# Kernel tuning notes

Hardware: AMD Instinct MI355X
Metric: run time of the kernel (lower is better)

## Reference

```python
import jax, jax.numpy as jnp
import numpy as np


def setup_inputs() -> dict:
    key = jax.random.key(0)
    k1, k2, k3, k4 = jax.random.split(key, 4)
    B, C = 32768, 10
    x = jax.random.normal(k1, (B, 1, 28, 28), dtype=jnp.float32)
    linear_weight = jax.random.normal(k2, (4 * 14 * 14 + 1 + 2, C), dtype=jnp.float32)
    linear_bias = jax.random.normal(k3, (C,), dtype=jnp.float32)
    sampler_weights = jax.random.normal(k4, (4,), dtype=jnp.float32)
    return {"x": x, "linear_weight": linear_weight, "linear_bias": linear_bias,
            "sampler_weights": sampler_weights}


def reference(x, linear_weight, linear_bias, sampler_weights):
    # Closed-form simulation of the 4-qubit circuits:
    # RY(t)|0> -> <Z>=cos(t); after CX(0,1): <Z1> = cos(t0)*cos(t1); CX(2,3) likewise.
    B = x.shape[0]
    # Extract non-overlapping 2x2 patches in row-major order -> (B, 196, 4)
    p = x[:, 0].reshape(B, 14, 2, 14, 2).transpose(0, 1, 3, 2, 4).reshape(B, 196, 4)
    c = jnp.cos(p)
    # quanvolution_circuit per patch: [cos a, cos a cos b, cos c, cos c cos d]
    feats = jnp.stack([c[..., 0], c[..., 0] * c[..., 1],
                       c[..., 2], c[..., 2] * c[..., 3]], axis=-1)  # (B,196,4)
    qfeat = feats.reshape(B, 784)
    # fully_connected_circuit on qfeat[:, :4]: mean of the four post-CX <Z>
    cf = jnp.cos(qfeat[:, :4])
    qfc = (cf[:, 0] + cf[:, 0] * cf[:, 1] + cf[:, 2] + cf[:, 2] * cf[:, 3]) / 4.0  # (B,)
    # sampler_circuit: sequential RY angles add on wires 0 and 1
    t0 = qfeat[:, 0] + sampler_weights[0] + sampler_weights[2]
    t1 = qfeat[:, 1] + sampler_weights[1] + sampler_weights[3]
    z0 = jnp.cos(t0)
    z1 = z0 * jnp.cos(t1)
    sampler = jax.nn.softmax(jnp.stack([z0, z1], axis=-1), axis=-1)  # (B,2)
    combined = jnp.concatenate([qfeat, qfc[:, None], sampler], axis=-1)  # (B,787)
    logits = combined @ linear_weight + linear_bias
    return jax.nn.log_softmax(logits, axis=-1)
```

## Files before the change

kernel.cpp:

```cpp
#include <hip/hip_runtime.h>


__global__ __launch_bounds__(256, 8)
void qml_k1(const float* __restrict__ x,
            const float* __restrict__ wm,
            float* __restrict__ part,
            float* __restrict__ qf,
            int B, int nblk)
{
    __shared__ float red[3][64 * 11];

    const int lane = threadIdx.x & 63;
    const int wv = __builtin_amdgcn_readfirstlane((int)(threadIdx.x >> 6));
    const int g = blockIdx.x;
    const int ps = blockIdx.y;

    int sample = g * 64 + lane;
    const bool s_ok = (sample < B);
    if (sample >= B) sample = B - 1;
    const float* __restrict__ xrow = x + (size_t)sample * 784;

    const int i = 2 * ps + (wv >> 1);
    const int j = 7 * (wv & 1);
    const int p0 = i * 14 + j;
    const int xoff = i * 56 + 2 * j;

    float acc[10];
#pragma unroll
    for (int c = 0; c < 10; ++c) acc[c] = 0.0f;

    float q0 = 0.f, q1 = 0.f, q2 = 0.f, q3 = 0.f;

#pragma unroll
    for (int t = 0; t < 7; ++t) {
        const float2 a01 = *(const float2*)(xrow + xoff + 2 * t);
        const float2 a23 = *(const float2*)(xrow + xoff + 28 + 2 * t);

        const float c0 = __cosf(a01.x);
        const float c1 = __cosf(a01.y);
        const float c2 = __cosf(a23.x);
        const float c3 = __cosf(a23.y);
        const float v0 = c0;
        const float v1 = c0 * c1;
        const float v2 = c2;
        const float v3 = c2 * c3;

        if (t == 0 && ps == 0 && wv == 0) { q0 = v0; q1 = v1; q2 = v2; q3 = v3; }

        const float* __restrict__ wr = wm + 40 * (p0 + t);
#pragma unroll
        for (int c = 0; c < 10; ++c)
            acc[c] += v0 * wr[c] + v1 * wr[10 + c] + v2 * wr[20 + c] + v3 * wr[30 + c];
    }

    if (ps == 0 && wv == 0 && s_ok) {
        float* __restrict__ qd = qf + 4 * (size_t)sample;
        qd[0] = q0; qd[1] = q1; qd[2] = q2; qd[3] = q3;
    }

    if (wv != 0) {
#pragma unroll
        for (int c = 0; c < 10; ++c) red[wv - 1][lane * 11 + c] = acc[c];
    }
    __syncthreads();

    if (wv == 0) {
        float* __restrict__ dst = part + ((size_t)(ps * nblk + g)) * 640 + lane * 10;
#pragma unroll
        for (int c = 0; c < 10; ++c)
            dst[c] = acc[c] + red[0][lane * 11 + c] + red[1][lane * 11 + c]
                            + red[2][lane * 11 + c];
    }
}

__global__ __launch_bounds__(640, 1)
void qml_k2(const float* __restrict__ part,
            const float* __restrict__ qf,
            const float* __restrict__ wm,
            const float* __restrict__ bias,
            const float* __restrict__ sw,
            float* __restrict__ out,
            int B, int nblk)
{
    __shared__ float lg[64 * 11];

    const int t = threadIdx.x;
    const int g = blockIdx.x;
    const int s = t / 10;
    const int c = t - 10 * s;

    float sum = 0.0f;
#pragma unroll
    for (int ps = 0; ps < 7; ++ps)
        sum += part[((size_t)(ps * nblk + g)) * 640 + t];

    int sample = g * 64 + s;
    const bool ok = (sample < B);
    if (sample >= B) sample = B - 1;

    const float* __restrict__ qr = qf + 4 * (size_t)sample;
    const float q0 = qr[0], q1 = qr[1], q2 = qr[2], q3 = qr[3];

    const float f0 = __cosf(q0), f1 = __cosf(q1);
    const float f2 = __cosf(q2), f3 = __cosf(q3);
    const float qfc = (f0 + f0 * f1 + f2 + f2 * f3) * 0.25f;

    const float t0 = q0 + sw[0] + sw[2];
    const float t1 = q1 + sw[1] + sw[3];
    const float z0 = __cosf(t0);
    const float z1 = z0 * __cosf(t1);
    const float e0 = __expf(z0);
    const float e1 = __expf(z1);
    const float inv = 1.0f / (e0 + e1);
    const float s0 = e0 * inv, s1 = e1 * inv;

    const float* __restrict__ wt = wm + 7840;
    const float logit = sum + bias[c] + qfc * wt[c] + s0 * wt[10 + c] + s1 * wt[20 + c];
    lg[s * 11 + c] = logit;
    __syncthreads();

    float m = -3.4e38f;
#pragma unroll
    for (int k = 0; k < 10; ++k) m = fmaxf(m, lg[s * 11 + k]);
    float ssum = 0.0f;
#pragma unroll
    for (int k = 0; k < 10; ++k) ssum += __expf(lg[s * 11 + k] - m);
    const float lse = __logf(ssum) + m;

    if (ok) out[(size_t)g * 640 + t] = logit - lse;
}

extern "C" void kernel_launch(void* const* d_in, const int* in_sizes, int n_in,
                              void* d_out, int out_size, void* d_ws, size_t ws_size,
                              hipStream_t stream) {
    const float* x    = (const float*)d_in[0];
    const float* w    = (const float*)d_in[1];
    const float* bias = (const float*)d_in[2];
    const float* sw   = (const float*)d_in[3];
    float* out = (float*)d_out;

    const int B = in_sizes[0] / 784;
    const int nblk = (B + 63) / 64;

    float* part = (float*)d_ws;
    float* qf   = part + (size_t)7 * nblk * 640;

    dim3 grid1(nblk, 7);
    qml_k1<<<grid1, 256, 0, stream>>>(x, w, part, qf, B, nblk);
    qml_k2<<<nblk, 640, 0, stream>>>(part, qf, w, bias, sw, out, B, nblk);
}
```

Measured before the change: 181.8 us.

## Stage input rows through swizzled LDS with coalesced loads and transpose partial layouts

Each block now loads its 64 samples' 4-row slab with coalesced float4 reads into XOR-swizzled shared memory, instead of per-lane strided float2 reads straight from global memory. The partial sums and the qf features are stored column-major so that writes and reads in both kernels coalesce. The second kernel is remapped to match, and an extra LDS pass produces the output row-major. This replaces uncoalesced global traffic, at the cost of 32KB of LDS per block and a lower occupancy hint (launch bounds 5 instead of 8).

Result: faster. 165.0 us (-9.3%).

```diff
diff --git a/kernel.cpp b/kernel.cpp
--- a/kernel.cpp
+++ b/kernel.cpp
@@ -1,75 +1,98 @@
 #include <hip/hip_runtime.h>
 
 
-__global__ __launch_bounds__(256, 8)
+__global__ __launch_bounds__(256, 5)
 void qml_k1(const float* __restrict__ x,
             const float* __restrict__ wm,
             float* __restrict__ part,
             float* __restrict__ qf,
             int B, int nblk)
 {
-    __shared__ float red[3][64 * 11];
+    __shared__ float lds[64 * 128];
 
-    const int lane = threadIdx.x & 63;
-    const int wv = __builtin_amdgcn_readfirstlane((int)(threadIdx.x >> 6));
+    const int t = threadIdx.x;
+    const int lane = t & 63;
+    const int wv = __builtin_amdgcn_readfirstlane((int)(t >> 6));
     const int g = blockIdx.x;
     const int ps = blockIdx.y;
 
-    int sample = g * 64 + lane;
-    const bool s_ok = (sample < B);
-    if (sample >= B) sample = B - 1;
-    const float* __restrict__ xrow = x + (size_t)sample * 784;
+    {
+        const int base_s = g * 64;
+#pragma unroll
+        for (int k = 0; k < 7; ++k) {
+            const int f = k * 256 + t;
+            const int s = f / 28;
+            const int c = f - 28 * s;
+            int sg = base_s + s; if (sg >= B) sg = B - 1;
+            const float4 v = *(const float4*)(x + (size_t)sg * 784 + ps * 112 + 4 * c);
+            const int m2 = (s & 15) << 1;
+            float* __restrict__ d0 = lds + s * 128 + ((4 * c) ^ m2);
+            float* __restrict__ d1 = lds + s * 128 + ((4 * c + 2) ^ m2);
+            *(float2*)d0 = make_float2(v.x, v.y);
+            *(float2*)d1 = make_float2(v.z, v.w);
+        }
+    }
+    __syncthreads();
 
-    const int i = 2 * ps + (wv >> 1);
-    const int j = 7 * (wv & 1);
-    const int p0 = i * 14 + j;
-    const int xoff = i * 56 + 2 * j;
+    const int i_loc = wv >> 1;
+    const int jbase = 7 * (wv & 1);
+    const int o_top = i_loc * 56 + 2 * jbase;
+    const int p0 = (2 * ps + i_loc) * 14 + jbase;
+    const int m2 = (lane & 15) << 1;
+    const float* __restrict__ row = lds + lane * 128;
 
     float acc[10];
 #pragma unroll
     for (int c = 0; c < 10; ++c) acc[c] = 0.0f;
-
     float q0 = 0.f, q1 = 0.f, q2 = 0.f, q3 = 0.f;
 
 #pragma unroll
-    for (int t = 0; t < 7; ++t) {
-        const float2 a01 = *(const float2*)(xrow + xoff + 2 * t);
-        const float2 a23 = *(const float2*)(xrow + xoff + 28 + 2 * t);
+    for (int tt = 0; tt < 7; ++tt) {
+        const int ot = o_top + 2 * tt;
+        const float2 a = *(const float2*)(row + (ot ^ m2));
+        const float2 b = *(const float2*)(row + ((ot + 28) ^ m2));
 
-        const float c0 = __cosf(a01.x);
-        const float c1 = __cosf(a01.y);
-        const float c2 = __cosf(a23.x);
-        const float c3 = __cosf(a23.y);
-        const float v0 = c0;
-        const float v1 = c0 * c1;
-        const float v2 = c2;
-        const float v3 = c2 * c3;
+        const float c0 = __cosf(a.x);
+        const float c1 = __cosf(a.y);
+        const float c2 = __cosf(b.x);
+        const float c3 = __cosf(b.y);
+        const float v0 = c0, v1 = c0 * c1, v2 = c2, v3 = c2 * c3;
 
-        if (t == 0 && ps == 0 && wv == 0) { q0 = v0; q1 = v1; q2 = v2; q3 = v3; }
+        if (ps == 0 && wv == 0 && tt == 0) { q0 = v0; q1 = v1; q2 = v2; q3 = v3; }
 
-        const float* __restrict__ wr = wm + 40 * (p0 + t);
+        const float* __restrict__ wr = wm + 40 * (p0 + tt);
 #pragma unroll
         for (int c = 0; c < 10; ++c)
             acc[c] += v0 * wr[c] + v1 * wr[10 + c] + v2 * wr[20 + c] + v3 * wr[30 + c];
     }
 
-    if (ps == 0 && wv == 0 && s_ok) {
-        float* __restrict__ qd = qf + 4 * (size_t)sample;
-        qd[0] = q0; qd[1] = q1; qd[2] = q2; qd[3] = q3;
-    }
+    __syncthreads();
 
     if (wv != 0) {
 #pragma unroll
-        for (int c = 0; c < 10; ++c) red[wv - 1][lane * 11 + c] = acc[c];
+        for (int c = 0; c < 10; ++c) lds[(wv - 1) * 704 + lane * 11 + c] = acc[c];
     }
     __syncthreads();
 
     if (wv == 0) {
-        float* __restrict__ dst = part + ((size_t)(ps * nblk + g)) * 640 + lane * 10;
 #pragma unroll
         for (int c = 0; c < 10; ++c)
-            dst[c] = acc[c] + red[0][lane * 11 + c] + red[1][lane * 11 + c]
-                            + red[2][lane * 11 + c];
+            acc[c] += lds[lane * 11 + c] + lds[704 + lane * 11 + c]
+                    + lds[1408 + lane * 11 + c];
+
+        float* __restrict__ dst = part + (size_t)(ps * nblk + g) * 640;
+#pragma unroll
+        for (int c = 0; c < 10; ++c) dst[c * 64 + lane] = acc[c];
+
+        if (ps == 0) {
+            const int sample = g * 64 + lane;
+            if (sample < B) {
+                qf[0 * (size_t)B + sample] = q0;
+                qf[1 * (size_t)B + sample] = q1;
+                qf[2 * (size_t)B + sample] = q2;
+                qf[3 * (size_t)B + sample] = q3;
+            }
+        }
     }
 }
 
@@ -86,20 +109,22 @@
 
     const int t = threadIdx.x;
     const int g = blockIdx.x;
-    const int s = t / 10;
-    const int c = t - 10 * s;
+    const int c = t >> 6;
+    const int s = t & 63;
 
     float sum = 0.0f;
 #pragma unroll
     for (int ps = 0; ps < 7; ++ps)
-        sum += part[((size_t)(ps * nblk + g)) * 640 + t];
+        sum += part[(size_t)(ps * nblk + g) * 640 + c * 64 + s];
 
     int sample = g * 64 + s;
     const bool ok = (sample < B);
     if (sample >= B) sample = B - 1;
 
-    const float* __restrict__ qr = qf + 4 * (size_t)sample;
-    const float q0 = qr[0], q1 = qr[1], q2 = qr[2], q3 = qr[3];
+    const float q0 = qf[0 * (size_t)B + sample];
+    const float q1 = qf[1 * (size_t)B + sample];
+    const float q2 = qf[2 * (size_t)B + sample];
+    const float q3 = qf[3 * (size_t)B + sample];
 
     const float f0 = __cosf(q0), f1 = __cosf(q1);
     const float f2 = __cosf(q2), f3 = __cosf(q3);
@@ -119,15 +144,18 @@
     lg[s * 11 + c] = logit;
     __syncthreads();
 
+    const int s2 = t / 10;
+    const int c2 = t - 10 * s2;
     float m = -3.4e38f;
 #pragma unroll
-    for (int k = 0; k < 10; ++k) m = fmaxf(m, lg[s * 11 + k]);
+    for (int k = 0; k < 10; ++k) m = fmaxf(m, lg[s2 * 11 + k]);
     float ssum = 0.0f;
 #pragma unroll
-    for (int k = 0; k < 10; ++k) ssum += __expf(lg[s * 11 + k] - m);
+    for (int k = 0; k < 10; ++k) ssum += __expf(lg[s2 * 11 + k] - m);
     const float lse = __logf(ssum) + m;
 
-    if (ok) out[(size_t)g * 640 + t] = logit - lse;
+    if (g * 64 + s2 < B)
+        out[(size_t)g * 640 + t] = lg[s2 * 11 + c2] - lse;
 }
 
 extern "C" void kernel_launch(void* const* d_in, const int* in_sizes, int n_in,
```
